# Kernel optimization log

Measured on AMD Instinct MI355X. Metric: run time of the kernel, lower is better.

Reference implementation:

```python
import jax, jax.numpy as jnp
import numpy as np

HEAD_DIM = 64
EMB_DIM = 768
BATCH = 4
SEQ = 4096

def setup_inputs() -> dict:
    key = jax.random.key(0)
    ks = jax.random.split(key, 7)
    s = 1.0 / np.sqrt(EMB_DIM)
    return {
        "X": jax.random.normal(ks[0], (BATCH, SEQ, EMB_DIM), dtype=jnp.float32),
        "Wq": jax.random.uniform(ks[1], (EMB_DIM, HEAD_DIM), jnp.float32, -s, s),
        "bq": jax.random.uniform(ks[2], (HEAD_DIM,), jnp.float32, -s, s),
        "Wk": jax.random.uniform(ks[3], (EMB_DIM, HEAD_DIM), jnp.float32, -s, s),
        "bk": jax.random.uniform(ks[4], (HEAD_DIM,), jnp.float32, -s, s),
        "Wv": jax.random.uniform(ks[5], (EMB_DIM, HEAD_DIM), jnp.float32, -s, s),
        "bv": jax.random.uniform(ks[6], (HEAD_DIM,), jnp.float32, -s, s),
    }

def reference(X, Wq, bq, Wk, bk, Wv, bv):
    # X: (B, S, E)
    B, S, E = X.shape
    q = X @ Wq + bq  # (B, S, D)
    k = X @ Wk + bk
    v = X @ Wv + bv
    scores = jnp.einsum("bsd,btd->bst", q, k)  # (B, S, S)
    # Original masks with -inf BEFORE scaling; -inf/sqrt(d) stays -inf,
    # so equivalent to: mask then scale.
    causal = jnp.tril(jnp.ones((S, S), dtype=bool))
    scores = jnp.where(causal, scores, -jnp.inf) / jnp.sqrt(jnp.float32(q.shape[-1]))
    w = jax.nn.softmax(scores, axis=-1)
    # dropout_rate = 0.0 (eval-equivalent): identity
    return jnp.einsum("bst,btd->bsd", w, v)
```

## Files before the change

kernel.cpp:

```cpp
#include <hip/hip_runtime.h>
#include <stdint.h>


#define QSCALE 0.18033688011112042f

using short4v = __attribute__((ext_vector_type(4))) short;
using short8v = __attribute__((ext_vector_type(8))) short;
using float4v = __attribute__((ext_vector_type(4))) float;
using uint4v  = __attribute__((ext_vector_type(4))) unsigned int;
typedef unsigned long long ull;
typedef unsigned short ushort;

#if __has_builtin(__builtin_amdgcn_exp2f)
#define EXP2F(x) __builtin_amdgcn_exp2f(x)
#else
#define EXP2F(x) exp2f(x)
#endif

__device__ __forceinline__ ushort f2b(float f) {
  union { float f; unsigned u; } cv; cv.f = f;
  unsigned u = cv.u;
  u += 0x7FFFu + ((u >> 16) & 1u);
  return (ushort)(u >> 16);
}

__global__ void wpack_kernel(const float* __restrict__ Wq, const float* __restrict__ bq,
                             const float* __restrict__ Wk, const float* __restrict__ bk,
                             const float* __restrict__ Wv, const float* __restrict__ bv,
                             ushort* __restrict__ Wt, float* __restrict__ bb) {
  __shared__ float tile[64 * 65];
  const int t = threadIdx.x;
  const int m = blockIdx.x % 3, e0 = (blockIdx.x / 3) * 64;
  const float* Wsrc = (m == 0) ? Wq : (m == 1) ? Wk : Wv;
  const float sc = (m == 0) ? QSCALE : 1.0f;
#pragma unroll
  for (int i = 0; i < 16; ++i) {
    int idx = i * 256 + t, n = idx & 63, el = idx >> 6;
    tile[el * 65 + n] = Wsrc[(size_t)(e0 + el) * 64 + n];
  }
  __syncthreads();
#pragma unroll
  for (int i = 0; i < 16; ++i) {
    int idx = i * 256 + t, el = idx & 63, n = idx >> 6;
    Wt[(size_t)(m * 64 + n) * 768 + e0 + el] = f2b(tile[el * 65 + n] * sc);
  }
  if (blockIdx.x == 0 && t < 192) {
    float bvv;
    if (t < 64)       bvv = bq[t] * QSCALE;
    else if (t < 128) bvv = bk[t - 64];
    else              bvv = bv[t - 128];
    bb[t] = bvv;
  }
}

__global__ __launch_bounds__(256) void proj_kernel(
    const float* __restrict__ X, const ushort* __restrict__ Wt,
    const float* __restrict__ bb,
    ushort* __restrict__ Qb, ushort* __restrict__ Kb, ushort* __restrict__ Vt) {
  __shared__ char lx[2][4096];
  const int t = threadIdx.x;
  const int wv = t >> 6, lane = t & 63, g = lane >> 4, r = lane & 15;
  const int row0 = blockIdx.x * 32;

  float4v acc[3][2];
#pragma unroll
  for (int ct = 0; ct < 3; ++ct) {
    float bias = bb[wv * 48 + ct * 16 + r];
#pragma unroll
    for (int rt = 0; rt < 2; ++rt) acc[ct][rt] = {bias, bias, bias, bias};
  }

  const int rr = t >> 3, sg = t & 7;
  const float* xbase = X + (size_t)(row0 + rr) * 768 + sg * 8;
  const ushort* wbase = Wt + (size_t)(wv * 48 + r) * 768 + g * 8;
  const int xoff = (rr * 128 + sg * 16) ^ ((rr & 7) << 4);

  float4v xh0, xh1, xn0, xn1;
  short8v wcur[6], wnxt[6];

  {
    xh0 = *(const float4v*)xbase;
    xh1 = *(const float4v*)(xbase + 4);
#pragma unroll
    for (int ct = 0; ct < 3; ++ct)
#pragma unroll
      for (int ks = 0; ks < 2; ++ks)
        wcur[ct * 2 + ks] = *(const short8v*)(wbase + ct * 16 * 768 + ks * 32);
    uint4v pk;
    pk[0] = f2b(xh0[0]) | ((unsigned)f2b(xh0[1]) << 16);
    pk[1] = f2b(xh0[2]) | ((unsigned)f2b(xh0[3]) << 16);
    pk[2] = f2b(xh1[0]) | ((unsigned)f2b(xh1[1]) << 16);
    pk[3] = f2b(xh1[2]) | ((unsigned)f2b(xh1[3]) << 16);
    *(uint4v*)(lx[0] + xoff) = pk;
    xh0 = *(const float4v*)(xbase + 64);
    xh1 = *(const float4v*)(xbase + 68);
  }
  __syncthreads();

#pragma unroll
  for (int kc = 0; kc < 12; ++kc) {
    if (kc + 2 < 12) {
      xn0 = *(const float4v*)(xbase + (kc + 2) * 64);
      xn1 = *(const float4v*)(xbase + (kc + 2) * 64 + 4);
    }
    if (kc + 1 < 12) {
#pragma unroll
      for (int ct = 0; ct < 3; ++ct)
#pragma unroll
        for (int ks = 0; ks < 2; ++ks)
          wnxt[ct * 2 + ks] =
              *(const short8v*)(wbase + ct * 16 * 768 + (kc + 1) * 64 + ks * 32);
    }
    short8v a[2][2];
#pragma unroll
    for (int rt = 0; rt < 2; ++rt)
#pragma unroll
      for (int ks = 0; ks < 2; ++ks) {
        int off = ((rt * 16 + r) * 128 + ks * 64 + g * 16) ^ ((r & 7) << 4);
        a[rt][ks] = *(const short8v*)(lx[kc & 1] + off);
      }
#pragma unroll
    for (int ct = 0; ct < 3; ++ct)
#pragma unroll
      for (int rt = 0; rt < 2; ++rt) {
        acc[ct][rt] = __builtin_amdgcn_mfma_f32_16x16x32_bf16(a[rt][0], wcur[ct * 2 + 0], acc[ct][rt], 0, 0, 0);
        acc[ct][rt] = __builtin_amdgcn_mfma_f32_16x16x32_bf16(a[rt][1], wcur[ct * 2 + 1], acc[ct][rt], 0, 0, 0);
      }
    if (kc + 1 < 12) {
      uint4v pk;
      pk[0] = f2b(xh0[0]) | ((unsigned)f2b(xh0[1]) << 16);
      pk[1] = f2b(xh0[2]) | ((unsigned)f2b(xh0[3]) << 16);
      pk[2] = f2b(xh1[0]) | ((unsigned)f2b(xh1[1]) << 16);
      pk[3] = f2b(xh1[2]) | ((unsigned)f2b(xh1[3]) << 16);
      *(uint4v*)(lx[(kc + 1) & 1] + xoff) = pk;
    }
    __syncthreads();
    xh0 = xn0; xh1 = xn1;
#pragma unroll
    for (int i = 0; i < 6; ++i) wcur[i] = wnxt[i];
  }
#pragma unroll
  for (int ct = 0; ct < 3; ++ct) {
    int n = wv * 48 + ct * 16 + r;
    int mtx = n >> 6, dl = n & 63;
#pragma unroll
    for (int rt = 0; rt < 2; ++rt) {
#pragma unroll
      for (int i = 0; i < 4; ++i) {
        int rg = row0 + rt * 16 + g * 4 + i;
        ushort hv = f2b(acc[ct][rt][i]);
        if (mtx == 0)      Qb[rg * 64 + dl] = hv;
        else if (mtx == 1) Kb[rg * 64 + dl] = hv;
        else               Vt[(size_t)(((rg >> 12) << 6) + dl) * 4096 + (rg & 4095)] = hv;
      }
    }
  }
}

__global__ __launch_bounds__(512) void attn_kernel(
    const ushort* __restrict__ Qb, const ushort* __restrict__ Kb,
    const ushort* __restrict__ Vt, float* __restrict__ pacc, float* __restrict__ pml) {
  __shared__ char lds[32768];
  char* lk = lds;
  char* lv = lds + 16384;
  const int t = threadIdx.x;
  const int wv = t >> 6, lane = t & 63, g = lane >> 4, r = lane & 15;
  const int bx = blockIdx.x;
  const int b = bx / 144;
  int rem = bx - b * 144;
  int g2 = 0;
  while (2 * (g2 + 1) * (g2 + 2) <= rem) ++g2;
  int rem2 = rem - 2 * g2 * (g2 + 1);
  int q_ = rem2 / (g2 + 1);
  const int st = 4 * g2 + q_;
  const int c = rem2 - q_ * (g2 + 1);

  const int s0 = c * 32;
  const int smax = min(32, 8 * st + 8 - s0);
  const int nm = smax >> 2;
  const int mysteps = min(8 * st + wv + 1 - s0, smax);
  const int dloc = 8 * st + wv - s0;

  const size_t qoff = ((size_t)(b * 4096 + st * 128 + wv * 16 + r)) * 64 + g * 8;
  const short8v qf0 = *(const short8v*)(Qb + qoff);
  const short8v qf1 = *(const short8v*)(Qb + qoff + 32);

  float4v acc[4];
#pragma unroll
  for (int dt = 0; dt < 4; ++dt) acc[dt] = {0.f, 0.f, 0.f, 0.f};
  float mrun = -3.0e38f, lsum = 0.f;

  const int kr = t >> 3, sg = t & 7;
  const ushort* ksrc = Kb + ((size_t)(b * 4096 + c * 512 + kr)) * 64 + sg * 8;
  const ushort* vsrc = Vt + ((size_t)(b * 64 + kr)) * 4096 + c * 512 + sg * 8;
  const int kwoff = (kr * 128 + sg * 16) ^ ((kr & 7) << 4);
  const int wsw = (kr >> 2) & 3;
  const int vwbase = (sg >> 1) * 2048 + kr * 32;
  const int vs0 = (((sg & 1) * 2) ^ wsw) * 8, vs1 = (((sg & 1) * 2 + 1) ^ wsw) * 8;

  uint4v kR1, vR1, kR2, vR2;
  auto stload = [&](int m, uint4v& kk, uint4v& vvv) {
    kk  = *(const uint4v*)(ksrc + (size_t)m * 64 * 64);
    vvv = *(const uint4v*)(vsrc + m * 64);
  };
  auto stwrite = [&](int bi, uint4v kk, uint4v vvv) {
    *(uint4v*)(lk + bi * 8192 + kwoff) = kk;
    char* vb = lv + bi * 8192 + vwbase;
    *(ull*)(vb + vs0) = (ull)vvv[0] | ((ull)vvv[1] << 32);
    *(ull*)(vb + vs1) = (ull)vvv[2] | ((ull)vvv[3] << 32);
  };

  auto micro = [&](int bi, int ks, bool masked) {
    const char* lkb = lk + bi * 8192;
    const char* lvb = lv + bi * 8192 + ks * 2048;
    const int krow = ks * 16 + r;
    const int ksw = (r & 7) << 4;
    const short8v k0 = *(const short8v*)(lkb + ((krow * 128 + g * 16) ^ ksw));
    const short8v k1 = *(const short8v*)(lkb + ((krow * 128 + g * 16 + 64) ^ ksw));
    float4v s = {0.f, 0.f, 0.f, 0.f};
    s = __builtin_amdgcn_mfma_f32_16x16x32_bf16(k0, qf0, s, 0, 0, 0);
    s = __builtin_amdgcn_mfma_f32_16x16x32_bf16(k1, qf1, s, 0, 0, 0);
    float u0 = s[0], u1 = s[1], u2 = s[2], u3 = s[3];
    if (masked) {
      int k4 = g << 2;
      u0 = (k4 + 0 <= r) ? u0 : -3.0e38f;
      u1 = (k4 + 1 <= r) ? u1 : -3.0e38f;
      u2 = (k4 + 2 <= r) ? u2 : -3.0e38f;
      u3 = (k4 + 3 <= r) ? u3 : -3.0e38f;
    }
    float tmax = fmaxf(fmaxf(u0, u1), fmaxf(u2, u3));
    tmax = fmaxf(tmax, __shfl_xor(tmax, 16));
    tmax = fmaxf(tmax, __shfl_xor(tmax, 32));
    float p0, p1, p2, p3;
    if (__all(tmax <= mrun)) {
      p0 = EXP2F(u0 - mrun); p1 = EXP2F(u1 - mrun);
      p2 = EXP2F(u2 - mrun); p3 = EXP2F(u3 - mrun);
      lsum += (p0 + p1) + (p2 + p3);
    } else {
      float mn = fmaxf(mrun, tmax);
      float rs = EXP2F(mrun - mn);
      mrun = mn;
      p0 = EXP2F(u0 - mn); p1 = EXP2F(u1 - mn);
      p2 = EXP2F(u2 - mn); p3 = EXP2F(u3 - mn);
      lsum = lsum * rs + ((p0 + p1) + (p2 + p3));
#pragma unroll
      for (int dt = 0; dt < 4; ++dt) acc[dt] *= rs;
    }
    short4v pf;
    pf[0] = (short)f2b(p0); pf[1] = (short)f2b(p1);
    pf[2] = (short)f2b(p2); pf[3] = (short)f2b(p3);
    const int vsl = (g ^ (r >> 2)) << 3;
#pragma unroll
    for (int dt = 0; dt < 4; ++dt) {
      const short4v vf = *(const short4v*)(lvb + (16 * dt + r) * 32 + vsl);
      acc[dt] = __builtin_amdgcn_mfma_f32_16x16x16bf16_1k(vf, pf, acc[dt], 0, 0, 0);
    }
  };

  stload(0, kR1, vR1);
  stwrite(0, kR1, vR1);
  if (nm > 1) stload(1, kR1, vR1);
  __syncthreads();

  for (int m = 0; m < nm; ++m) {
    if (m + 2 < nm) stload(m + 2, kR2, vR2);
    const int nl = mysteps - m * 4;
    const int bi = m & 1;
    if (nl > 0) micro(bi, 0, m * 4 + 0 == dloc);
    if (nl > 1) micro(bi, 1, m * 4 + 1 == dloc);
    if (nl > 2) micro(bi, 2, m * 4 + 2 == dloc);
    if (nl > 3) micro(bi, 3, m * 4 + 3 == dloc);
    if (m + 1 < nm) stwrite((m + 1) & 1, kR1, vR1);
    __syncthreads();
    kR1 = kR2; vR1 = vR2;
  }

  lsum += __shfl_xor(lsum, 16);
  lsum += __shfl_xor(lsum, 32);

  const int slot = bx;
  const int prow = wv * 16 + r;
  if (g == 0) {
    pml[slot * 256 + prow * 2 + 0] = mrun;
    pml[slot * 256 + prow * 2 + 1] = lsum;
  }
  float* pp = pacc + (size_t)slot * 8192 + prow * 64 + g * 4;
#pragma unroll
  for (int dt = 0; dt < 4; ++dt)
    *(float4v*)(pp + dt * 16) = acc[dt];
}

__global__ __launch_bounds__(256) void combine_kernel(
    const float* __restrict__ pacc, const float* __restrict__ pml,
    float* __restrict__ out) {
  const int bx = blockIdx.x;
  const int rq = bx & 3, st = (bx >> 2) & 31, b = bx >> 7;
  const int g2 = st >> 2, nc = g2 + 1;
  const int sb = b * 144 + 2 * g2 * (g2 + 1) + (st - 4 * g2) * nc;
  const int t = threadIdx.x;
  const int row = rq * 32 + (t >> 3);
  const int d0 = (t & 7) * 8;

  float M = -3.0e38f;
  for (int p = 0; p < nc; ++p)
    M = fmaxf(M, pml[(sb + p) * 256 + row * 2]);
  float denom = 0.f;
  float4v v0 = {0.f, 0.f, 0.f, 0.f}, v1 = {0.f, 0.f, 0.f, 0.f};
  for (int p = 0; p < nc; ++p) {
    float m = pml[(sb + p) * 256 + row * 2];
    float l = pml[(sb + p) * 256 + row * 2 + 1];
    float wgt = EXP2F(m - M);
    denom += l * wgt;
    const float* ap = pacc + (size_t)(sb + p) * 8192 + row * 64 + d0;
    v0 += *(const float4v*)ap * wgt;
    v1 += *(const float4v*)(ap + 4) * wgt;
  }
  float inv = 1.0f / denom;
  float* op = out + ((size_t)(b * 4096 + st * 128 + row)) * 64 + d0;
  *(float4v*)op = v0 * inv;
  *(float4v*)(op + 4) = v1 * inv;
}

extern "C" void kernel_launch(void* const* d_in, const int* in_sizes, int n_in,
                              void* d_out, int out_size, void* d_ws, size_t ws_size,
                              hipStream_t stream) {
  const float* X  = (const float*)d_in[0];
  const float* Wq = (const float*)d_in[1];
  const float* bq = (const float*)d_in[2];
  const float* Wk = (const float*)d_in[3];
  const float* bk = (const float*)d_in[4];
  const float* Wv = (const float*)d_in[5];
  const float* bv = (const float*)d_in[6];
  float* out = (float*)d_out;

  ushort* Qb = (ushort*)d_ws;
  ushort* Kb = Qb + 4 * 4096 * 64;
  ushort* Vt = Kb + 4 * 4096 * 64;
  ushort* Wt = Vt + 4 * 4096 * 64;
  float* bb  = (float*)(Wt + 192 * 768);
  float* pml  = bb + 256;
  float* pacc = pml + 576 * 256;

  wpack_kernel<<<36, 256, 0, stream>>>(Wq, bq, Wk, bk, Wv, bv, Wt, bb);
  proj_kernel<<<512, 256, 0, stream>>>(X, Wt, bb, Qb, Kb, Vt);
  attn_kernel<<<576, 512, 0, stream>>>(Qb, Kb, Vt, pacc, pml);
  combine_kernel<<<512, 256, 0, stream>>>(pacc, pml, out);
}
```

Baseline: 158.9 us.

## Halve attention query tile, store partials in fp16, drop LDS staging in projection

```diff
diff --git a/kernel.cpp b/kernel.cpp
--- a/kernel.cpp
+++ b/kernel.cpp
@@ -22,6 +22,14 @@
   unsigned u = cv.u;
   u += 0x7FFFu + ((u >> 16) & 1u);
   return (ushort)(u >> 16);
+}
+__device__ __forceinline__ ushort f2h(float f) {
+  union { ushort u; _Float16 h; } cv; cv.h = (_Float16)f;
+  return cv.u;
+}
+__device__ __forceinline__ float h2f(unsigned u16) {
+  union { ushort u; _Float16 h; } cv; cv.u = (ushort)u16;
+  return (float)cv.h;
 }
 
 __global__ void wpack_kernel(const float* __restrict__ Wq, const float* __restrict__ bq,
@@ -53,11 +61,10 @@
   }
 }
 
-__global__ __launch_bounds__(256) void proj_kernel(
+__global__ __launch_bounds__(256, 4) void proj_kernel(
     const float* __restrict__ X, const ushort* __restrict__ Wt,
     const float* __restrict__ bb,
     ushort* __restrict__ Qb, ushort* __restrict__ Kb, ushort* __restrict__ Vt) {
-  __shared__ char lx[2][4096];
   const int t = threadIdx.x;
   const int wv = t >> 6, lane = t & 63, g = lane >> 4, r = lane & 15;
   const int row0 = blockIdx.x * 32;
@@ -70,74 +77,37 @@
     for (int rt = 0; rt < 2; ++rt) acc[ct][rt] = {bias, bias, bias, bias};
   }
 
-  const int rr = t >> 3, sg = t & 7;
-  const float* xbase = X + (size_t)(row0 + rr) * 768 + sg * 8;
-  const ushort* wbase = Wt + (size_t)(wv * 48 + r) * 768 + g * 8;
-  const int xoff = (rr * 128 + sg * 16) ^ ((rr & 7) << 4);
-
-  float4v xh0, xh1, xn0, xn1;
-  short8v wcur[6], wnxt[6];
-
-  {
-    xh0 = *(const float4v*)xbase;
-    xh1 = *(const float4v*)(xbase + 4);
-#pragma unroll
-    for (int ct = 0; ct < 3; ++ct)
-#pragma unroll
-      for (int ks = 0; ks < 2; ++ks)
-        wcur[ct * 2 + ks] = *(const short8v*)(wbase + ct * 16 * 768 + ks * 32);
-    uint4v pk;
-    pk[0] = f2b(xh0[0]) | ((unsigned)f2b(xh0[1]) << 16);
-    pk[1] = f2b(xh0[2]) | ((unsigned)f2b(xh0[3]) << 16);
-    pk[2] = f2b(xh1[0]) | ((unsigned)f2b(xh1[1]) << 16);
-    pk[3] = f2b(xh1[2]) | ((unsigned)f2b(xh1[3]) << 16);
-    *(uint4v*)(lx[0] + xoff) = pk;
-    xh0 = *(const float4v*)(xbase + 64);
-    xh1 = *(const float4v*)(xbase + 68);
-  }
-  __syncthreads();
-
-#pragma unroll
+  const float* xb = X + (size_t)(row0 + r) * 768 + g * 8;
+  const ushort* wb = Wt + (size_t)(wv * 48 + r) * 768 + g * 8;
+
+#pragma unroll 2
   for (int kc = 0; kc < 12; ++kc) {
-    if (kc + 2 < 12) {
-      xn0 = *(const float4v*)(xbase + (kc + 2) * 64);
-      xn1 = *(const float4v*)(xbase + (kc + 2) * 64 + 4);
-    }
-    if (kc + 1 < 12) {
-#pragma unroll
-      for (int ct = 0; ct < 3; ++ct)
-#pragma unroll
-        for (int ks = 0; ks < 2; ++ks)
-          wnxt[ct * 2 + ks] =
-              *(const short8v*)(wbase + ct * 16 * 768 + (kc + 1) * 64 + ks * 32);
-    }
-    short8v a[2][2];
+    const int k0 = kc * 64;
+    short8v af[2][2];
 #pragma unroll
     for (int rt = 0; rt < 2; ++rt)
 #pragma unroll
       for (int ks = 0; ks < 2; ++ks) {
-        int off = ((rt * 16 + r) * 128 + ks * 64 + g * 16) ^ ((r & 7) << 4);
-        a[rt][ks] = *(const short8v*)(lx[kc & 1] + off);
+        const float* xp = xb + rt * 16 * 768 + k0 + ks * 32;
+        float4v x0 = *(const float4v*)xp;
+        float4v x1 = *(const float4v*)(xp + 4);
+        short8v v;
+        v[0] = (short)f2b(x0[0]); v[1] = (short)f2b(x0[1]);
+        v[2] = (short)f2b(x0[2]); v[3] = (short)f2b(x0[3]);
+        v[4] = (short)f2b(x1[0]); v[5] = (short)f2b(x1[1]);
+        v[6] = (short)f2b(x1[2]); v[7] = (short)f2b(x1[3]);
+        af[rt][ks] = v;
       }
 #pragma unroll
-    for (int ct = 0; ct < 3; ++ct)
+    for (int ct = 0; ct < 3; ++ct) {
+      short8v b0 = *(const short8v*)(wb + ct * 16 * 768 + k0);
+      short8v b1 = *(const short8v*)(wb + ct * 16 * 768 + k0 + 32);
 #pragma unroll
       for (int rt = 0; rt < 2; ++rt) {
-        acc[ct][rt] = __builtin_amdgcn_mfma_f32_16x16x32_bf16(a[rt][0], wcur[ct * 2 + 0], acc[ct][rt], 0, 0, 0);
-        acc[ct][rt] = __builtin_amdgcn_mfma_f32_16x16x32_bf16(a[rt][1], wcur[ct * 2 + 1], acc[ct][rt], 0, 0, 0);
+        acc[ct][rt] = __builtin_amdgcn_mfma_f32_16x16x32_bf16(af[rt][0], b0, acc[ct][rt], 0, 0, 0);
+        acc[ct][rt] = __builtin_amdgcn_mfma_f32_16x16x32_bf16(af[rt][1], b1, acc[ct][rt], 0, 0, 0);
       }
-    if (kc + 1 < 12) {
-      uint4v pk;
-      pk[0] = f2b(xh0[0]) | ((unsigned)f2b(xh0[1]) << 16);
-      pk[1] = f2b(xh0[2]) | ((unsigned)f2b(xh0[3]) << 16);
-      pk[2] = f2b(xh1[0]) | ((unsigned)f2b(xh1[1]) << 16);
-      pk[3] = f2b(xh1[2]) | ((unsigned)f2b(xh1[3]) << 16);
-      *(uint4v*)(lx[(kc + 1) & 1] + xoff) = pk;
-    }
-    __syncthreads();
-    xh0 = xn0; xh1 = xn1;
-#pragma unroll
-    for (int i = 0; i < 6; ++i) wcur[i] = wnxt[i];
+    }
   }
 #pragma unroll
   for (int ct = 0; ct < 3; ++ct) {
@@ -157,31 +127,33 @@
   }
 }
 
-__global__ __launch_bounds__(512) void attn_kernel(
+__global__ __launch_bounds__(256) void attn_kernel(
     const ushort* __restrict__ Qb, const ushort* __restrict__ Kb,
-    const ushort* __restrict__ Vt, float* __restrict__ pacc, float* __restrict__ pml) {
+    const ushort* __restrict__ Vt, ushort* __restrict__ pacc,
+    float* __restrict__ pml) {
   __shared__ char lds[32768];
   char* lk = lds;
   char* lv = lds + 16384;
   const int t = threadIdx.x;
   const int wv = t >> 6, lane = t & 63, g = lane >> 4, r = lane & 15;
   const int bx = blockIdx.x;
-  const int b = bx / 144;
-  int rem = bx - b * 144;
-  int g2 = 0;
-  while (2 * (g2 + 1) * (g2 + 2) <= rem) ++g2;
-  int rem2 = rem - 2 * g2 * (g2 + 1);
-  int q_ = rem2 / (g2 + 1);
-  const int st = 4 * g2 + q_;
-  const int c = rem2 - q_ * (g2 + 1);
+  const int b = bx / 288;
+  const int rem = bx - b * 288;
+  int a = 0;
+  while (4 * (a + 1) * (a + 2) <= rem) ++a;
+  const int rem2 = rem - 4 * a * (a + 1);
+  const int m_ = rem2 / (a + 1);
+  const int c = rem2 - m_ * (a + 1);
+  const int st = 8 * a + m_;
 
   const int s0 = c * 32;
-  const int smax = min(32, 8 * st + 8 - s0);
+  const int smax = min(32, 4 * st + 4 - s0);
   const int nm = smax >> 2;
-  const int mysteps = min(8 * st + wv + 1 - s0, smax);
-  const int dloc = 8 * st + wv - s0;
-
-  const size_t qoff = ((size_t)(b * 4096 + st * 128 + wv * 16 + r)) * 64 + g * 8;
+  const int qt = 4 * st + wv;
+  const int mysteps = min(qt + 1 - s0, smax);
+  const int dloc = qt - s0;
+
+  const size_t qoff = ((size_t)(b * 4096 + st * 64 + wv * 16 + r)) * 64 + g * 8;
   const short8v qf0 = *(const short8v*)(Qb + qoff);
   const short8v qf1 = *(const short8v*)(Qb + qoff + 32);
 
@@ -190,33 +162,41 @@
   for (int dt = 0; dt < 4; ++dt) acc[dt] = {0.f, 0.f, 0.f, 0.f};
   float mrun = -3.0e38f, lsum = 0.f;
 
-  const int kr = t >> 3, sg = t & 7;
-  const ushort* ksrc = Kb + ((size_t)(b * 4096 + c * 512 + kr)) * 64 + sg * 8;
-  const ushort* vsrc = Vt + ((size_t)(b * 64 + kr)) * 4096 + c * 512 + sg * 8;
-  const int kwoff = (kr * 128 + sg * 16) ^ ((kr & 7) << 4);
-  const int wsw = (kr >> 2) & 3;
-  const int vwbase = (sg >> 1) * 2048 + kr * 32;
-  const int vs0 = (((sg & 1) * 2) ^ wsw) * 8, vs1 = (((sg & 1) * 2 + 1) ^ wsw) * 8;
-
-  uint4v kR1, vR1, kR2, vR2;
-  auto stload = [&](int m, uint4v& kk, uint4v& vvv) {
-    kk  = *(const uint4v*)(ksrc + (size_t)m * 64 * 64);
-    vvv = *(const uint4v*)(vsrc + m * 64);
+  const int kr = t >> 2, sq = t & 3;
+  const ushort* ksrc = Kb + ((size_t)(b * 4096 + c * 512 + kr)) * 64 + sq * 16;
+  const ushort* vsrc = Vt + ((size_t)(b * 64 + kr)) * 4096 + c * 512 + sq * 16;
+  const int ksw = (kr & 7) << 4;
+  const int kwo0 = (kr * 128 + sq * 32) ^ ksw;
+  const int kwo1 = (kr * 128 + sq * 32 + 16) ^ ksw;
+  const int vwb = sq * 2048 + kr * 32;
+  const int sx = ((kr >> 2) & 3) ^ sq;
+
+  uint4v kA0, kA1, vA0, vA1, kB0, kB1, vB0, vB1;
+  auto stload = [&](int m, uint4v& k0, uint4v& k1, uint4v& v0, uint4v& v1) {
+    const ushort* kp = ksrc + (size_t)m * 64 * 64;
+    k0 = *(const uint4v*)kp;
+    k1 = *(const uint4v*)(kp + 8);
+    const ushort* vp = vsrc + m * 64;
+    v0 = *(const uint4v*)vp;
+    v1 = *(const uint4v*)(vp + 8);
   };
-  auto stwrite = [&](int bi, uint4v kk, uint4v vvv) {
-    *(uint4v*)(lk + bi * 8192 + kwoff) = kk;
-    char* vb = lv + bi * 8192 + vwbase;
-    *(ull*)(vb + vs0) = (ull)vvv[0] | ((ull)vvv[1] << 32);
-    *(ull*)(vb + vs1) = (ull)vvv[2] | ((ull)vvv[3] << 32);
+  auto stwrite = [&](int bi, uint4v k0, uint4v k1, uint4v v0, uint4v v1) {
+    *(uint4v*)(lk + bi * 8192 + kwo0) = k0;
+    *(uint4v*)(lk + bi * 8192 + kwo1) = k1;
+    char* vb = lv + bi * 8192 + vwb;
+    *(ull*)(vb + ((0 ^ sx) & 3) * 8) = (ull)v0[0] | ((ull)v0[1] << 32);
+    *(ull*)(vb + ((1 ^ sx) & 3) * 8) = (ull)v0[2] | ((ull)v0[3] << 32);
+    *(ull*)(vb + ((2 ^ sx) & 3) * 8) = (ull)v1[0] | ((ull)v1[1] << 32);
+    *(ull*)(vb + ((3 ^ sx) & 3) * 8) = (ull)v1[2] | ((ull)v1[3] << 32);
   };
 
   auto micro = [&](int bi, int ks, bool masked) {
     const char* lkb = lk + bi * 8192;
     const char* lvb = lv + bi * 8192 + ks * 2048;
     const int krow = ks * 16 + r;
-    const int ksw = (r & 7) << 4;
-    const short8v k0 = *(const short8v*)(lkb + ((krow * 128 + g * 16) ^ ksw));
-    const short8v k1 = *(const short8v*)(lkb + ((krow * 128 + g * 16 + 64) ^ ksw));
+    const int rsw = (r & 7) << 4;
+    const short8v k0 = *(const short8v*)(lkb + ((krow * 128 + g * 16) ^ rsw));
+    const short8v k1 = *(const short8v*)(lkb + ((krow * 128 + g * 16 + 64) ^ rsw));
     float4v s = {0.f, 0.f, 0.f, 0.f};
     s = __builtin_amdgcn_mfma_f32_16x16x32_bf16(k0, qf0, s, 0, 0, 0);
     s = __builtin_amdgcn_mfma_f32_16x16x32_bf16(k1, qf1, s, 0, 0, 0);
@@ -249,7 +229,7 @@
     short4v pf;
     pf[0] = (short)f2b(p0); pf[1] = (short)f2b(p1);
     pf[2] = (short)f2b(p2); pf[3] = (short)f2b(p3);
-    const int vsl = (g ^ (r >> 2)) << 3;
+    const int vsl = ((g ^ (r >> 2) ^ ks) & 3) << 3;
 #pragma unroll
     for (int dt = 0; dt < 4; ++dt) {
       const short4v vf = *(const short4v*)(lvb + (16 * dt + r) * 32 + vsl);
@@ -257,22 +237,22 @@
     }
   };
 
-  stload(0, kR1, vR1);
-  stwrite(0, kR1, vR1);
-  if (nm > 1) stload(1, kR1, vR1);
+  stload(0, kA0, kA1, vA0, vA1);
+  stwrite(0, kA0, kA1, vA0, vA1);
+  if (nm > 1) stload(1, kA0, kA1, vA0, vA1);
   __syncthreads();
 
   for (int m = 0; m < nm; ++m) {
-    if (m + 2 < nm) stload(m + 2, kR2, vR2);
+    if (m + 2 < nm) stload(m + 2, kB0, kB1, vB0, vB1);
     const int nl = mysteps - m * 4;
     const int bi = m & 1;
     if (nl > 0) micro(bi, 0, m * 4 + 0 == dloc);
     if (nl > 1) micro(bi, 1, m * 4 + 1 == dloc);
     if (nl > 2) micro(bi, 2, m * 4 + 2 == dloc);
     if (nl > 3) micro(bi, 3, m * 4 + 3 == dloc);
-    if (m + 1 < nm) stwrite((m + 1) & 1, kR1, vR1);
+    if (m + 1 < nm) stwrite((m + 1) & 1, kA0, kA1, vA0, vA1);
     __syncthreads();
-    kR1 = kR2; vR1 = vR2;
+    kA0 = kB0; kA1 = kB1; vA0 = vB0; vA1 = vB1;
   }
 
   lsum += __shfl_xor(lsum, 16);
@@ -281,42 +261,47 @@
   const int slot = bx;
   const int prow = wv * 16 + r;
   if (g == 0) {
-    pml[slot * 256 + prow * 2 + 0] = mrun;
-    pml[slot * 256 + prow * 2 + 1] = lsum;
-  }
-  float* pp = pacc + (size_t)slot * 8192 + prow * 64 + g * 4;
-#pragma unroll
-  for (int dt = 0; dt < 4; ++dt)
-    *(float4v*)(pp + dt * 16) = acc[dt];
-}
-
-__global__ __launch_bounds__(256) void combine_kernel(
-    const float* __restrict__ pacc, const float* __restrict__ pml,
+    pml[slot * 128 + prow * 2 + 0] = mrun;
+    pml[slot * 128 + prow * 2 + 1] = lsum;
+  }
+  ushort* pp = pacc + (size_t)slot * 4096 + prow * 64;
+#pragma unroll
+  for (int dt = 0; dt < 4; ++dt) {
+    ull pk = (ull)f2h(acc[dt][0]) | ((ull)f2h(acc[dt][1]) << 16) |
+             ((ull)f2h(acc[dt][2]) << 32) | ((ull)f2h(acc[dt][3]) << 48);
+    *(ull*)(pp + dt * 16 + g * 4) = pk;
+  }
+}
+
+__global__ __launch_bounds__(64) void combine_kernel(
+    const ushort* __restrict__ pacc, const float* __restrict__ pml,
     float* __restrict__ out) {
   const int bx = blockIdx.x;
-  const int rq = bx & 3, st = (bx >> 2) & 31, b = bx >> 7;
-  const int g2 = st >> 2, nc = g2 + 1;
-  const int sb = b * 144 + 2 * g2 * (g2 + 1) + (st - 4 * g2) * nc;
+  const int rq = bx & 7, st = (bx >> 3) & 63, b = bx >> 9;
+  const int a = st >> 3, nc = a + 1;
+  const int sb = b * 288 + 4 * a * (a + 1) + (st & 7) * (a + 1);
   const int t = threadIdx.x;
-  const int row = rq * 32 + (t >> 3);
+  const int row = rq * 8 + (t >> 3);
   const int d0 = (t & 7) * 8;
 
   float M = -3.0e38f;
   for (int p = 0; p < nc; ++p)
-    M = fmaxf(M, pml[(sb + p) * 256 + row * 2]);
+    M = fmaxf(M, pml[(sb + p) * 128 + row * 2]);
   float denom = 0.f;
   float4v v0 = {0.f, 0.f, 0.f, 0.f}, v1 = {0.f, 0.f, 0.f, 0.f};
   for (int p = 0; p < nc; ++p) {
-    float m = pml[(sb + p) * 256 + row * 2];
-    float l = pml[(sb + p) * 256 + row * 2 + 1];
+    float m = pml[(sb + p) * 128 + row * 2];
+    float l = pml[(sb + p) * 128 + row * 2 + 1];
     float wgt = EXP2F(m - M);
     denom += l * wgt;
-    const float* ap = pacc + (size_t)(sb + p) * 8192 + row * 64 + d0;
-    v0 += *(const float4v*)ap * wgt;
-    v1 += *(const float4v*)(ap + 4) * wgt;
+    uint4v hv = *(const uint4v*)(pacc + (size_t)(sb + p) * 4096 + row * 64 + d0);
+    v0[0] += wgt * h2f(hv[0] & 0xffff); v0[1] += wgt * h2f(hv[0] >> 16);
+    v0[2] += wgt * h2f(hv[1] & 0xffff); v0[3] += wgt * h2f(hv[1] >> 16);
+    v1[0] += wgt * h2f(hv[2] & 0xffff); v1[1] += wgt * h2f(hv[2] >> 16);
+    v1[2] += wgt * h2f(hv[3] & 0xffff); v1[3] += wgt * h2f(hv[3] >> 16);
   }
   float inv = 1.0f / denom;
-  float* op = out + ((size_t)(b * 4096 + st * 128 + row)) * 64 + d0;
+  float* op = out + ((size_t)(b * 4096 + st * 64 + row)) * 64 + d0;
   *(float4v*)op = v0 * inv;
   *(float4v*)(op + 4) = v1 * inv;
 }
@@ -339,10 +324,10 @@
   ushort* Wt = Vt + 4 * 4096 * 64;
   float* bb  = (float*)(Wt + 192 * 768);
   float* pml  = bb + 256;
-  float* pacc = pml + 576 * 256;
+  ushort* pacc = (ushort*)(pml + 1152 * 128);
 
   wpack_kernel<<<36, 256, 0, stream>>>(Wq, bq, Wk, bk, Wv, bv, Wt, bb);
   proj_kernel<<<512, 256, 0, stream>>>(X, Wt, bb, Qb, Kb, Vt);
-  attn_kernel<<<576, 512, 0, stream>>>(Qb, Kb, Vt, pacc, pml);
-  combine_kernel<<<512, 256, 0, stream>>>(pacc, pml, out);
-}
+  attn_kernel<<<1152, 256, 0, stream>>>(Qb, Kb, Vt, pacc, pml);
+  combine_kernel<<<2048, 64, 0, stream>>>(pacc, pml, out);
+}
```

Result: slower. 183.1 us (+15.2%).
